# Kernel optimization log

Measured on AMD Instinct MI355X. Metric: run time of the kernel, lower is better.

Reference implementation:

```python
import jax, jax.numpy as jnp
import numpy as np
from jax import lax

B, T, C = 2, 1024, 2048
H, N = 32, 64
LAYER_ID, N_LAYER = 1, 24
EPS = 1e-5 * 64.0  # 1e-5 * head_size_divisor**2, divisor=8
RESCALE_T = 256.0 * 0.7  # bf16_limit * 0.7


def setup_inputs():
    key = jax.random.key(0)
    ks = jax.random.split(key, 16)
    r01 = LAYER_ID / (N_LAYER - 1)
    r10 = 1.0 - LAYER_ID / N_LAYER
    ddd = np.arange(C, dtype=np.float64) / C
    pw = lambda p: jnp.asarray(1.0 - ddd ** p, jnp.float32)
    n = np.arange(C, dtype=np.float64)
    decay = -7.0 + 5.0 * (n / (C - 1)) ** (0.85 + r01 ** 0.5)
    sc = lambda k, shp, s: jax.random.normal(k, shp, jnp.float32) * s
    return {
        'x': sc(ks[0], (B, T, C), 1.0),
        'v_first': sc(ks[1], (B, T, C), 1.0),
        'x_r': pw(0.2 * r10), 'x_w': pw(0.9 * r10),
        'x_k': jnp.asarray(1.0 - (ddd ** (0.9 * r10) + 0.4 * r01), jnp.float32),
        'x_v': jnp.asarray(1.0 - (ddd ** (0.4 * r10) + 0.6 * r01), jnp.float32),
        'x_a': pw(0.9 * r10), 'x_g': pw(0.2 * r10),
        'w0': jnp.asarray(decay + 0.5, jnp.float32),
        'w1': sc(ks[2], (C, 64), 0.02), 'w2': sc(ks[3], (64, C), 0.02),
        'a0': jnp.zeros((C,), jnp.float32),
        'a1': sc(ks[4], (C, 64), 0.02), 'a2': sc(ks[5], (64, C), 0.02),
        'v0': jnp.ones((C,), jnp.float32),
        'v1': sc(ks[6], (C, 32), 0.02), 'v2': sc(ks[7], (32, C), 0.02),
        'g1': sc(ks[8], (C, 128), 0.02), 'g2': sc(ks[9], (128, C), 0.02),
        'k_k': jnp.full((C,), 0.85, jnp.float32),
        'k_a': jnp.ones((C,), jnp.float32),
        'r_k': sc(ks[10], (H, N), 0.05),
        'W_r': sc(ks[11], (C, C), C ** -0.5),
        'W_k': sc(ks[12], (C, C), C ** -0.5),
        'W_v': sc(ks[13], (C, C), C ** -0.5),
        'W_o': sc(ks[14], (C, C), C ** -0.5),
        'ln_w': jnp.ones((C,), jnp.float32),
        'ln_b': jnp.zeros((C,), jnp.float32),
    }


def wkv7(r, w, k, v, a, b):
    # RWKV-7 per-head linear state recurrence: S <- S*diag(w) + S a b^T + v k^T; out = S r
    Bsz, Tlen, Cd = r.shape
    to = lambda t: t.reshape(Bsz, Tlen, H, N).transpose(1, 0, 2, 3)  # (T,B,H,N)
    rr, kk, vv, aa, bb = map(to, (r, k, v, a, b))
    ww = jnp.exp(-jnp.exp(to(w)))  # decay in (0,1); w <= -0.5 guaranteed upstream

    def step(S, xs):
        rt, wt, kt, vt, at, bt = xs
        sa = jnp.einsum('bhij,bhj->bhi', S, at)
        S = S * wt[:, :, None, :] + sa[..., None] * bt[:, :, None, :] + vt[..., None] * kt[:, :, None, :]
        return S, jnp.einsum('bhij,bhj->bhi', S, rt)

    S0 = jnp.zeros((Bsz, H, N, N), r.dtype)
    _, out = lax.scan(step, S0, (rr, ww, kk, vv, aa, bb))
    return out.transpose(1, 0, 2, 3).reshape(Bsz, Tlen, Cd)


def reference(x, v_first, x_r, x_w, x_k, x_v, x_a, x_g, w0, w1, w2, a0, a1, a2,
              v0, v1, v2, g1, g2, k_k, k_a, r_k, W_r, W_k, W_v, W_o, ln_w, ln_b):
    # token shift (ZeroPad2d((0,0,1,-1)))
    xx = jnp.concatenate([jnp.zeros_like(x[:, :1]), x[:, :-1]], axis=1) - x
    xr = x + xx * x_r; xw = x + xx * x_w; xk = x + xx * x_k
    xv = x + xx * x_v; xa = x + xx * x_a; xg = x + xx * x_g
    r = xr @ W_r.T
    w = -jax.nn.softplus(-(w0 + jnp.tanh(xw @ w1) @ w2)) - 0.5  # soft clamp to (-inf,-0.5]
    k = xk @ W_k.T
    v = xv @ W_v.T
    # layer_id > 0: value residual gated toward v_first (with max-abs rescales)
    v1p = xv @ v1
    v1p = v1p / jnp.maximum(jnp.max(jnp.abs(v1p)), 1.0)
    v2p = v1p @ v2
    v2p = v2p / jnp.maximum(jnp.max(jnp.abs(v2p)), 1.0)
    gate = jax.nn.sigmoid(jnp.clip(v0 + v2p, -16.0, 16.0))
    vd = v_first - v
    vd = vd / jnp.maximum(jnp.max(jnp.abs(vd)), 1.0)
    v = v + vd * gate
    a = jax.nn.sigmoid(a0 + (xa @ a1) @ a2)
    g = jax.nn.sigmoid(xg @ g1) @ g2
    kk = (k * k_k).reshape(B, T, H, N)
    kk = (kk / jnp.maximum(jnp.linalg.norm(kk, axis=-1, keepdims=True), 1e-12)).reshape(B, T, C)
    k = k * (1.0 + (a - 1.0) * k_a)
    y = wkv7(r, w, k, v, -kk, kk * a)
    needs_rescale = jnp.max(jnp.abs(y)) > RESCALE_T
    # GroupNorm: H groups of size N
    yg = y.reshape(B, T, H, N)
    mu = yg.mean(-1, keepdims=True)
    var = yg.var(-1, keepdims=True)
    y = ((yg - mu) / jnp.sqrt(var + EPS)).reshape(B, T, C) * ln_w + ln_b
    y = y + ((r.reshape(B, T, H, N) * k.reshape(B, T, H, N) * r_k).sum(-1, keepdims=True)
             * v.reshape(B, T, H, N)).reshape(B, T, C)
    y = (y * g) @ W_o.T
    y = jnp.where(needs_rescale, y * 0.5, y)
    v_first_out = jnp.where(needs_rescale, v_first * 0.5, v_first)
    return y, v_first_out
```

## Files before the change

### kernel.cpp

```cpp
#include <hip/hip_runtime.h>
#include <hip/hip_bf16.h>

#define ELq 4194304
#define Cq 2048
#define Tq 1024
#define Hq 32
#define Mq 2048

typedef __attribute__((ext_vector_type(8))) short bf16x8;
typedef __attribute__((ext_vector_type(4))) float f32x4;

__device__ __forceinline__ unsigned short f2bu(float f) {
  union { float f; unsigned u; } v; v.f = f;
  unsigned r = v.u + 0x7fffu + ((v.u >> 16) & 1u);
  return (unsigned short)(r >> 16);
}
__device__ __forceinline__ float b2f(unsigned short u) {
  union { unsigned u; float f; } v; v.u = ((unsigned)u) << 16;
  return v.f;
}
__device__ __forceinline__ void gl_lds16(const void* g, void* l) {
  __builtin_amdgcn_global_load_lds((const __attribute__((address_space(1))) unsigned int*)g,
                                   (__attribute__((address_space(3))) unsigned int*)l, 16, 0, 0);
}

template<int CTRL>
__device__ __forceinline__ float dpp_add(float x) {
  int t = __builtin_amdgcn_update_dpp(0, __builtin_bit_cast(int, x), CTRL, 0xF, 0xF, true);
  return x + __builtin_bit_cast(float, t);
}

struct ConvJob { const float* src; unsigned short* dst; int rows, cols, trans; };
struct ConvJobs { ConvJob j[12]; };

__global__ void k_conv(ConvJobs jobs) {
  ConvJob jb = jobs.j[blockIdx.z];
  int n = jb.rows * jb.cols;
  if (!jb.trans) {
    int n4 = n >> 2;
    for (int i = blockIdx.x * blockDim.x + threadIdx.x; i < n4; i += gridDim.x * blockDim.x) {
      float4 v = ((const float4*)jb.src)[i];
      ushort4 o;
      o.x = f2bu(v.x); o.y = f2bu(v.y); o.z = f2bu(v.z); o.w = f2bu(v.w);
      ((ushort4*)jb.dst)[i] = o;
    }
  } else {
    for (int i = blockIdx.x * blockDim.x + threadIdx.x; i < n; i += gridDim.x * blockDim.x) {
      int col = i / jb.rows;
      int row = i - col * jb.rows;
      jb.dst[i] = f2bu(jb.src[(size_t)row * jb.cols + col]);
    }
  }
}

__global__ void k_zero(unsigned int* p) { if (threadIdx.x < 8) p[threadIdx.x] = 0u; }

__global__ void k_prologue(const float* __restrict__ x,
    const float* __restrict__ mr, const float* __restrict__ mw, const float* __restrict__ mk,
    const float* __restrict__ mv, const float* __restrict__ ma, const float* __restrict__ mg,
    unsigned short* __restrict__ xr, unsigned short* __restrict__ xw, unsigned short* __restrict__ xk,
    unsigned short* __restrict__ xv, unsigned short* __restrict__ xa, unsigned short* __restrict__ xg)
{
  int i4 = blockIdx.x * 256 + threadIdx.x;
  if (i4 >= ELq / 4) return;
  int i = i4 << 2;
  float4 xc = *(const float4*)(x + i);
  int t = (i >> 11) & (Tq - 1);
  float4 xp = make_float4(0.f, 0.f, 0.f, 0.f);
  if (t) xp = *(const float4*)(x + i - Cq);
  float4 dx = make_float4(xp.x - xc.x, xp.y - xc.y, xp.z - xc.z, xp.w - xc.w);
  int c = i & (Cq - 1);
  auto mix = [&](const float* __restrict__ m, unsigned short* __restrict__ o) {
    float4 mm = *(const float4*)(m + c);
    ushort4 u;
    u.x = f2bu(xc.x + dx.x * mm.x); u.y = f2bu(xc.y + dx.y * mm.y);
    u.z = f2bu(xc.z + dx.z * mm.z); u.w = f2bu(xc.w + dx.w * mm.w);
    *(ushort4*)(o + i) = u;
  };
  mix(mr, xr); mix(mw, xw); mix(mk, xk); mix(mv, xv); mix(ma, xa); mix(mg, xg);
}

struct GJob {
  const unsigned short* A; const unsigned short* B;
  const float* bias; float* Cf; unsigned short* Cb;
  unsigned int* amax; const float* aux;
  int K; int ld; int epi;
};
struct GJobs { GJob j[4]; };

__device__ __forceinline__ void epi_store(int epi, float v, size_t o,
    float* Cf, unsigned short* Cb, const float* bias, const float* aux, int col, float& lmax)
{
  switch (epi) {
    case 0: Cf[o] = v; break;
    case 1: Cf[o] = v + bias[col]; break;
    case 2: Cf[o] = 1.f / (1.f + expf(-(v + bias[col]))); break;
    case 4: Cb[o] = f2bu(v); break;
    case 7: lmax = fmaxf(lmax, fabsf(v)); Cf[o] = v; break;
    case 9: lmax = fmaxf(lmax, fabsf(aux[o] - v)); Cf[o] = v; break;
  }
}

__global__ __launch_bounds__(256, 2) void k_gemm128(GJobs jobs) {
  GJob jb = jobs.j[blockIdx.z];
  __shared__ __align__(16) unsigned short As[128 * 32];
  __shared__ __align__(16) unsigned short Bs[128 * 32];
  __shared__ float sred[4];
  const int tid = threadIdx.x, lane = tid & 63, wid = tid >> 6;
  const int wr = wid >> 1, wc = wid & 1;
  const int lin = blockIdx.y * 16 + blockIdx.x;
  const int swz = (lin & 7) * 32 + (lin >> 3);
  const int m0 = (swz >> 4) * 128, n0 = (swz & 15) * 128;
  const int K = jb.K, ld = jb.ld;
  const unsigned short* A = jb.A; const unsigned short* B = jb.B;
  f32x4 acc[4][4] = {};
  for (int k0 = 0; k0 < K; k0 += 32) {
    #pragma unroll
    for (int i = 0; i < 2; ++i) {
      int cw = wid * 64 + i * 256;
      int c = cw + lane;
      int row = c >> 2, q = c & 3;
      gl_lds16(A + (size_t)(m0 + row) * ld + k0 + q * 8, &As[cw * 8]);
      gl_lds16(B + (size_t)(n0 + row) * ld + k0 + q * 8, &Bs[cw * 8]);
    }
    __syncthreads();
    const int kg = (lane >> 4) * 8;
    bf16x8 af[4], bq[4];
    #pragma unroll
    for (int mi = 0; mi < 4; ++mi)
      af[mi] = *(const bf16x8*)&As[(wr * 64 + mi * 16 + (lane & 15)) * 32 + kg];
    #pragma unroll
    for (int ni = 0; ni < 4; ++ni)
      bq[ni] = *(const bf16x8*)&Bs[(wc * 64 + ni * 16 + (lane & 15)) * 32 + kg];
    #pragma unroll
    for (int mi = 0; mi < 4; ++mi)
      #pragma unroll
      for (int ni = 0; ni < 4; ++ni)
        acc[mi][ni] = __builtin_amdgcn_mfma_f32_16x16x32_bf16(af[mi], bq[ni], acc[mi][ni], 0, 0, 0);
    __syncthreads();
  }
  float lmax = 0.f;
  #pragma unroll
  for (int mi = 0; mi < 4; ++mi)
    #pragma unroll
    for (int ni = 0; ni < 4; ++ni) {
      int col = n0 + wc * 64 + ni * 16 + (lane & 15);
      int row = m0 + wr * 64 + mi * 16 + ((lane >> 4) << 2);
      #pragma unroll
      for (int q = 0; q < 4; ++q)
        epi_store(jb.epi, acc[mi][ni][q], (size_t)(row + q) * 2048 + col,
                  jb.Cf, jb.Cb, jb.bias, jb.aux, col, lmax);
    }
  if (jb.epi == 7 || jb.epi == 9) {
    #pragma unroll
    for (int o = 32; o; o >>= 1) lmax = fmaxf(lmax, __shfl_xor(lmax, o));
    if (lane == 0) sred[wid] = lmax;
    __syncthreads();
    if (tid == 0)
      atomicMax(jb.amax, __float_as_uint(fmaxf(fmaxf(sred[0], sred[1]), fmaxf(sred[2], sred[3]))));
  }
}

template<int TBN>
__global__ __launch_bounds__(256, 2) void k_gemmN_sk(GJob jb) {
  __shared__ __align__(16) unsigned short As[128 * 32];
  __shared__ __align__(16) unsigned short Bs[TBN * 32];
  const int tid = threadIdx.x, lane = tid & 63, wid = tid >> 6;
  const int m0 = blockIdx.x * 128;
  const int koff = blockIdx.y * 256;
  const int ld = jb.ld;
  constexpr int NF = TBN / 16;
  const unsigned short* A = jb.A + koff;
  const unsigned short* B = jb.B + koff;
  float* out = jb.Cf + (size_t)blockIdx.y * (2048 * TBN);
  f32x4 acc[2][NF] = {};
  for (int k0 = 0; k0 < 256; k0 += 32) {
    for (int cw = wid * 64; cw < 512; cw += 256) {
      int c = cw + lane; int row = c >> 2, q = c & 3;
      gl_lds16(A + (size_t)(m0 + row) * ld + k0 + q * 8, &As[cw * 8]);
    }
    for (int cw = wid * 64; cw < TBN * 4; cw += 256) {
      int c = cw + lane; int row = c >> 2, q = c & 3;
      gl_lds16(B + (size_t)row * ld + k0 + q * 8, &Bs[cw * 8]);
    }
    __syncthreads();
    const int kg = (lane >> 4) * 8;
    bf16x8 af[2], bq[NF];
    #pragma unroll
    for (int mi = 0; mi < 2; ++mi)
      af[mi] = *(const bf16x8*)&As[(wid * 32 + mi * 16 + (lane & 15)) * 32 + kg];
    #pragma unroll
    for (int ni = 0; ni < NF; ++ni)
      bq[ni] = *(const bf16x8*)&Bs[(ni * 16 + (lane & 15)) * 32 + kg];
    #pragma unroll
    for (int mi = 0; mi < 2; ++mi)
      #pragma unroll
      for (int ni = 0; ni < NF; ++ni)
        acc[mi][ni] = __builtin_amdgcn_mfma_f32_16x16x32_bf16(af[mi], bq[ni], acc[mi][ni], 0, 0, 0);
    __syncthreads();
  }
  #pragma unroll
  for (int mi = 0; mi < 2; ++mi)
    #pragma unroll
    for (int ni = 0; ni < NF; ++ni) {
      int col = ni * 16 + (lane & 15);
      int row = m0 + wid * 32 + mi * 16 + ((lane >> 4) << 2);
      #pragma unroll
      for (int q = 0; q < 4; ++q)
        out[(size_t)(row + q) * TBN + col] = acc[mi][ni][q];
    }
}

__global__ void k_skepi(const float* __restrict__ pw, const float* __restrict__ pa,
                        const float* __restrict__ pv, const float* __restrict__ pg,
                        unsigned short* __restrict__ hw, unsigned short* __restrict__ ha,
                        unsigned short* __restrict__ hv, unsigned short* __restrict__ hg,
                        unsigned int* __restrict__ amax) {
  int i = blockIdx.x * 256 + threadIdx.x;
  const float* src; unsigned short* dst; int stride, mode, loc;
  if (i < 131072)      { src = pw; dst = hw; stride = 131072; mode = 0; loc = i; }
  else if (i < 262144) { src = pa; dst = ha; stride = 131072; mode = 1; loc = i - 131072; }
  else if (i < 327680) { src = pv; dst = hv; stride = 65536;  mode = 2; loc = i - 262144; }
  else                 { src = pg; dst = hg; stride = 262144; mode = 3; loc = i - 327680; }
  float s = 0.f;
  #pragma unroll
  for (int sp = 0; sp < 8; ++sp) s += src[loc + (size_t)sp * stride];
  float lmax = 0.f, o;
  switch (mode) {
    case 0: o = tanhf(s); break;
    case 1: o = s; break;
    case 2: o = s; lmax = fabsf(s); break;
    default: o = 1.f / (1.f + expf(-s)); break;
  }
  dst[loc] = f2bu(o);
  #pragma unroll
  for (int of = 32; of; of >>= 1) lmax = fmaxf(lmax, __shfl_xor(lmax, of));
  if ((threadIdx.x & 63) == 0 && lmax > 0.f) atomicMax(amax, __float_as_uint(lmax));
}

__global__ __launch_bounds__(256) void k_vprep(float* __restrict__ v, const float* __restrict__ vf,
    const float* __restrict__ z, const float* __restrict__ v0c, const unsigned int* __restrict__ sc,
    float* __restrict__ k, float* __restrict__ w, float* __restrict__ asig, float* __restrict__ kkout,
    const float* __restrict__ kkw, const float* __restrict__ kaw) {
  int wid = threadIdx.x >> 6, lane = threadIdx.x & 63;
  int idx = blockIdx.x * 4 + wid;
  size_t off = (size_t)idx * 64 + lane;
  int c = ((idx & (Hq - 1)) << 6) | lane;
  float m1 = fmaxf(__uint_as_float(sc[0]), 1.f);
  float m2 = fmaxf(__uint_as_float(sc[1]) / m1, 1.f);
  float mvd = fmaxf(__uint_as_float(sc[2]), 1.f);
  float gx = v0c[c] + z[off] / (m1 * m2);
  gx = fminf(fmaxf(gx, -16.f), 16.f);
  float gate = 1.f / (1.f + expf(-gx));
  float vr = v[off];
  v[off] = vr + (vf[off] - vr) * (gate / mvd);
  float kr = k[off];
  float kkv = kr * kkw[c];
  float ss = kkv * kkv;
  #pragma unroll
  for (int o = 32; o; o >>= 1) ss += __shfl_xor(ss, o);
  float kkn = kkv / fmaxf(sqrtf(ss), 1e-12f);
  float as = asig[off];
  kkout[off] = -kkn;
  asig[off] = kkn * as;
  k[off] = kr * (1.f + (as - 1.f) * kaw[c]);
  float wl = w[off];
  float wlog = -log1pf(expf(-wl)) - 0.5f;
  w[off] = expf(-expf(wlog));
}

struct SRg { float4 r0, r1, w0, w1, k0, k1, a0, a1, b0, b1; float v; };

__device__ __forceinline__ void ld_g(SRg& R,
    const float* __restrict__ rS, const float* __restrict__ wS, const float* __restrict__ kS,
    const float* __restrict__ vS, const float* __restrict__ aS, const float* __restrict__ bS,
    size_t sb, int cq8, int row) {
  R.r0 = *(const float4*)(rS + sb + cq8); R.r1 = *(const float4*)(rS + sb + cq8 + 4);
  R.w0 = *(const float4*)(wS + sb + cq8); R.w1 = *(const float4*)(wS + sb + cq8 + 4);
  R.k0 = *(const float4*)(kS + sb + cq8); R.k1 = *(const float4*)(kS + sb + cq8 + 4);
  R.a0 = *(const float4*)(aS + sb + cq8); R.a1 = *(const float4*)(aS + sb + cq8 + 4);
  R.b0 = *(const float4*)(bS + sb + cq8); R.b1 = *(const float4*)(bS + sb + cq8 + 4);
  R.v  = vS[sb + row];
}

__device__ __forceinline__ void wkv_step(const SRg& R, float S[8], float& ymx,
    float* __restrict__ y, size_t yoff, int lane) {
  float sa = (S[0]*R.a0.x + S[1]*R.a0.y) + (S[2]*R.a0.z + S[3]*R.a0.w)
           + (S[4]*R.a1.x + S[5]*R.a1.y) + (S[6]*R.a1.z + S[7]*R.a1.w);
  sa = dpp_add<0xB1>(sa);
  sa = dpp_add<0x4E>(sa);
  sa = dpp_add<0x141>(sa);
  float vi = R.v;
  float s0 = S[0]*R.w0.x + (sa*R.b0.x + vi*R.k0.x);
  float s1 = S[1]*R.w0.y + (sa*R.b0.y + vi*R.k0.y);
  float s2 = S[2]*R.w0.z + (sa*R.b0.z + vi*R.k0.z);
  float s3 = S[3]*R.w0.w + (sa*R.b0.w + vi*R.k0.w);
  float s4 = S[4]*R.w1.x + (sa*R.b1.x + vi*R.k1.x);
  float s5 = S[5]*R.w1.y + (sa*R.b1.y + vi*R.k1.y);
  float s6 = S[6]*R.w1.z + (sa*R.b1.z + vi*R.k1.z);
  float s7 = S[7]*R.w1.w + (sa*R.b1.w + vi*R.k1.w);
  S[0]=s0; S[1]=s1; S[2]=s2; S[3]=s3; S[4]=s4; S[5]=s5; S[6]=s6; S[7]=s7;
  float yp = (s0*R.r0.x + s1*R.r0.y) + (s2*R.r0.z + s3*R.r0.w)
           + (s4*R.r1.x + s5*R.r1.y) + (s6*R.r1.z + s7*R.r1.w);
  yp = dpp_add<0xB1>(yp);
  yp = dpp_add<0x4E>(yp);
  yp = dpp_add<0x141>(yp);
  if ((lane & 7) == 0) {
    y[yoff] = yp;
    ymx = fmaxf(ymx, fabsf(yp));
  }
}

__global__ __launch_bounds__(64, 1) void k_wkv(
    const float* __restrict__ rS, const float* __restrict__ wS, const float* __restrict__ kS,
    const float* __restrict__ vS, const float* __restrict__ aS, const float* __restrict__ bS,
    float* __restrict__ y, unsigned int* __restrict__ ymax) {
  const int lane = threadIdx.x;
  const int bh = blockIdx.x & 63;
  const int rq = blockIdx.x >> 6;
  const int row = rq * 8 + (lane >> 3);
  const int cq8 = (lane & 7) * 8;
  float S[8];
  #pragma unroll
  for (int q = 0; q < 8; ++q) S[q] = 0.f;
  const size_t base0 = (size_t)(bh >> 5) * Tq * Cq + (size_t)(bh & 31) * 64;

  SRg R0, R1, R2, R3;
  ld_g(R0, rS, wS, kS, vS, aS, bS, base0,            cq8, row);
  ld_g(R1, rS, wS, kS, vS, aS, bS, base0 + Cq,       cq8, row);
  ld_g(R2, rS, wS, kS, vS, aS, bS, base0 + 2 * Cq,   cq8, row);
  ld_g(R3, rS, wS, kS, vS, aS, bS, base0 + 3 * Cq,   cq8, row);

  float ymx = 0.f;
  for (int t = 0; t < Tq; t += 4) {
    int t4 = (t + 4 < Tq) ? t + 4 : Tq - 1;
    int t5 = (t + 5 < Tq) ? t + 5 : Tq - 1;
    int t6 = (t + 6 < Tq) ? t + 6 : Tq - 1;
    int t7 = (t + 7 < Tq) ? t + 7 : Tq - 1;
    wkv_step(R0, S, ymx, y, base0 + (size_t)t * Cq + row, lane);
    ld_g(R0, rS, wS, kS, vS, aS, bS, base0 + (size_t)t4 * Cq, cq8, row);
    wkv_step(R1, S, ymx, y, base0 + (size_t)(t + 1) * Cq + row, lane);
    ld_g(R1, rS, wS, kS, vS, aS, bS, base0 + (size_t)t5 * Cq, cq8, row);
    wkv_step(R2, S, ymx, y, base0 + (size_t)(t + 2) * Cq + row, lane);
    ld_g(R2, rS, wS, kS, vS, aS, bS, base0 + (size_t)t6 * Cq, cq8, row);
    wkv_step(R3, S, ymx, y, base0 + (size_t)(t + 3) * Cq + row, lane);
    ld_g(R3, rS, wS, kS, vS, aS, bS, base0 + (size_t)t7 * Cq, cq8, row);
  }
  #pragma unroll
  for (int o = 32; o; o >>= 1) ymx = fmaxf(ymx, __shfl_xor(ymx, o));
  if (lane == 0) atomicMax(ymax, __float_as_uint(ymx));
}

__global__ __launch_bounds__(256) void k_epi1(const float* __restrict__ y, const float* __restrict__ r,
    const float* __restrict__ k, const float* __restrict__ v, const unsigned short* __restrict__ g,
    const float* __restrict__ lnw, const float* __restrict__ lnb, const float* __restrict__ rk,
    unsigned short* __restrict__ yg) {
  int wid = threadIdx.x >> 6, lane = threadIdx.x & 63;
  int idx = blockIdx.x * 4 + wid;
  size_t off = (size_t)idx * 64 + lane;
  int c = ((idx & (Hq - 1)) << 6) | lane;
  float yv = y[off];
  float s = yv;
  #pragma unroll
  for (int o = 32; o; o >>= 1) s += __shfl_xor(s, o);
  float mu = s * (1.f / 64.f);
  float d = yv - mu;
  float vs = d * d;
  #pragma unroll
  for (int o = 32; o; o >>= 1) vs += __shfl_xor(vs, o);
  float yn = d / sqrtf(vs * (1.f / 64.f) + 6.4e-4f);
  float yo = yn * lnw[c] + lnb[c];
  float bon = r[off] * k[off] * rk[c];
  #pragma unroll
  for (int o = 32; o; o >>= 1) bon += __shfl_xor(bon, o);
  yo += bon * v[off];
  yg[off] = f2bu(yo * b2f(g[off]));
}

__global__ void k_wo_fin(const float* __restrict__ p0, const float* __restrict__ p1,
                         const unsigned int* __restrict__ sc, float* __restrict__ out) {
  int i = blockIdx.x * 256 + threadIdx.x;
  if (i >= ELq / 4) return;
  float s = (__uint_as_float(sc[3]) > 179.2f) ? 0.5f : 1.f;
  float4 a = ((const float4*)p0)[i];
  float4 b = ((const float4*)p1)[i];
  ((float4*)out)[i] = make_float4((a.x + b.x) * s, (a.y + b.y) * s,
                                  (a.z + b.z) * s, (a.w + b.w) * s);
}

__global__ void k_vout(const float* __restrict__ vf, const unsigned int* __restrict__ sc,
                       float* __restrict__ out) {
  int i = blockIdx.x * 256 + threadIdx.x;
  if (i >= ELq) return;
  float s = (__uint_as_float(sc[3]) > 179.2f) ? 0.5f : 1.f;
  out[i] = vf[i] * s;
}

extern "C" void kernel_launch(void* const* d_in, const int* in_sizes, int n_in,
                              void* d_out, int out_size, void* d_ws, size_t ws_size,
                              hipStream_t stream) {
  const float* x      = (const float*)d_in[0];
  const float* vfirst = (const float*)d_in[1];
  const float* x_r = (const float*)d_in[2];
  const float* x_w = (const float*)d_in[3];
  const float* x_k = (const float*)d_in[4];
  const float* x_v = (const float*)d_in[5];
  const float* x_a = (const float*)d_in[6];
  const float* x_g = (const float*)d_in[7];
  const float* w0 = (const float*)d_in[8];
  const float* w1 = (const float*)d_in[9];
  const float* w2 = (const float*)d_in[10];
  const float* a0 = (const float*)d_in[11];
  const float* a1 = (const float*)d_in[12];
  const float* a2 = (const float*)d_in[13];
  const float* v0 = (const float*)d_in[14];
  const float* v1 = (const float*)d_in[15];
  const float* v2 = (const float*)d_in[16];
  const float* g1 = (const float*)d_in[17];
  const float* g2 = (const float*)d_in[18];
  const float* k_k = (const float*)d_in[19];
  const float* k_a = (const float*)d_in[20];
  const float* r_k = (const float*)d_in[21];
  const float* W_r = (const float*)d_in[22];
  const float* W_k = (const float*)d_in[23];
  const float* W_v = (const float*)d_in[24];
  const float* W_o = (const float*)d_in[25];
  const float* lnw = (const float*)d_in[26];
  const float* lnb = (const float*)d_in[27];

  char* ws = (char*)d_ws;
  size_t off = 0;
  auto alloc = [&](size_t bytes) -> void* {
    void* p = ws + off; off += (bytes + 255) & ~(size_t)255; return p;
  };
  unsigned int* scal = (unsigned int*)alloc(256);
  float* kbuf  = (float*)alloc((size_t)ELq * 4);
  float* vbuf  = (float*)alloc((size_t)ELq * 4);
  float* wbuf  = (float*)alloc((size_t)ELq * 4);
  float* abuf  = (float*)alloc((size_t)ELq * 4);
  float* kkbuf = (float*)alloc((size_t)ELq * 4);
  float* ybuf  = (float*)alloc((size_t)ELq * 4);
  unsigned short* xrb = (unsigned short*)alloc((size_t)ELq * 2);
  unsigned short* xwb = (unsigned short*)alloc((size_t)ELq * 2);
  unsigned short* xkb = (unsigned short*)alloc((size_t)ELq * 2);
  unsigned short* xvb = (unsigned short*)alloc((size_t)ELq * 2);
  unsigned short* xab = (unsigned short*)alloc((size_t)ELq * 2);
  unsigned short* xgb = (unsigned short*)alloc((size_t)ELq * 2);
  unsigned short* gbuf = (unsigned short*)alloc((size_t)ELq * 2);
  unsigned short* ygb  = (unsigned short*)alloc((size_t)ELq * 2);
  unsigned short* WrB = (unsigned short*)alloc((size_t)ELq * 2);
  unsigned short* WkB = (unsigned short*)alloc((size_t)ELq * 2);
  unsigned short* WvB = (unsigned short*)alloc((size_t)ELq * 2);
  unsigned short* WoB = (unsigned short*)alloc((size_t)ELq * 2);
  unsigned short* w1T = (unsigned short*)alloc(64 * 2048 * 2);
  unsigned short* a1T = (unsigned short*)alloc(64 * 2048 * 2);
  unsigned short* v1T = (unsigned short*)alloc(32 * 2048 * 2);
  unsigned short* g1T = (unsigned short*)alloc(128 * 2048 * 2);
  unsigned short* w2T = (unsigned short*)alloc(2048 * 64 * 2);
  unsigned short* a2T = (unsigned short*)alloc(2048 * 64 * 2);
  unsigned short* v2T = (unsigned short*)alloc(2048 * 32 * 2);
  unsigned short* g2T = (unsigned short*)alloc(2048 * 128 * 2);
  unsigned short* hwb = (unsigned short*)alloc((size_t)Mq * 64 * 2);
  unsigned short* hab = (unsigned short*)alloc((size_t)Mq * 64 * 2);
  unsigned short* hvb = (unsigned short*)alloc((size_t)Mq * 32 * 2);
  unsigned short* hgb = (unsigned short*)alloc((size_t)Mq * 128 * 2);
  float* pskw = (float*)alloc((size_t)8 * Mq * 64 * 4);
  float* pska = (float*)alloc((size_t)8 * Mq * 64 * 4);
  float* pskv = (float*)alloc((size_t)8 * Mq * 32 * 4);
  float* pskg = (float*)alloc((size_t)8 * Mq * 128 * 4);
  float* rbuf = (float*)d_out;
  float* zbuf = (float*)d_out + ELq;
  float* yout = (float*)d_out;
  float* vfout = (float*)d_out + ELq;
  float* pWo0 = (float*)xrb;
  float* pWo1 = pWo0 + ELq;

  k_zero<<<1, 64, 0, stream>>>(scal);

  ConvJobs cj;
  cj.j[0]  = {W_r, WrB, Cq, Cq, 0};
  cj.j[1]  = {W_k, WkB, Cq, Cq, 0};
  cj.j[2]  = {W_v, WvB, Cq, Cq, 0};
  cj.j[3]  = {W_o, WoB, Cq, Cq, 0};
  cj.j[4]  = {w1, w1T, 2048, 64, 1};
  cj.j[5]  = {a1, a1T, 2048, 64, 1};
  cj.j[6]  = {v1, v1T, 2048, 32, 1};
  cj.j[7]  = {g1, g1T, 2048, 128, 1};
  cj.j[8]  = {w2, w2T, 64, 2048, 1};
  cj.j[9]  = {a2, a2T, 64, 2048, 1};
  cj.j[10] = {v2, v2T, 32, 2048, 1};
  cj.j[11] = {g2, g2T, 128, 2048, 1};
  k_conv<<<dim3(1024, 1, 12), 256, 0, stream>>>(cj);

  k_prologue<<<ELq / 1024, 256, 0, stream>>>(x, x_r, x_w, x_k, x_v, x_a, x_g,
                                             xrb, xwb, xkb, xvb, xab, xgb);

  GJobs g1j;
  g1j.j[0] = {xrb, WrB, nullptr, rbuf, nullptr, nullptr, nullptr, 2048, 2048, 0};
  g1j.j[1] = {xkb, WkB, nullptr, kbuf, nullptr, nullptr, nullptr, 2048, 2048, 0};
  g1j.j[2] = {xvb, WvB, nullptr, vbuf, nullptr, scal + 2, vfirst, 2048, 2048, 9};
  g1j.j[3] = g1j.j[0];
  k_gemm128<<<dim3(16, 16, 3), 256, 0, stream>>>(g1j);

  GJob jw = {xwb, w1T, nullptr, pskw, nullptr, nullptr, nullptr, 256, 2048, 0};
  k_gemmN_sk<64><<<dim3(16, 8), 256, 0, stream>>>(jw);
  GJob ja = {xab, a1T, nullptr, pska, nullptr, nullptr, nullptr, 256, 2048, 0};
  k_gemmN_sk<64><<<dim3(16, 8), 256, 0, stream>>>(ja);
  GJob jv = {xvb, v1T, nullptr, pskv, nullptr, nullptr, nullptr, 256, 2048, 0};
  k_gemmN_sk<32><<<dim3(16, 8), 256, 0, stream>>>(jv);
  GJob jg = {xgb, g1T, nullptr, pskg, nullptr, nullptr, nullptr, 256, 2048, 0};
  k_gemmN_sk<128><<<dim3(16, 8), 256, 0, stream>>>(jg);
  k_skepi<<<2304, 256, 0, stream>>>(pskw, pska, pskv, pskg, hwb, hab, hvb, hgb, scal + 0);

  GJobs g3j;
  g3j.j[0] = {hwb, w2T, w0, wbuf, nullptr, nullptr, nullptr, 64, 64, 1};
  g3j.j[1] = {hab, a2T, a0, abuf, nullptr, nullptr, nullptr, 64, 64, 2};
  g3j.j[2] = {hvb, v2T, nullptr, zbuf, nullptr, scal + 1, nullptr, 32, 32, 7};
  g3j.j[3] = {hgb, g2T, nullptr, nullptr, gbuf, nullptr, nullptr, 128, 128, 4};
  k_gemm128<<<dim3(16, 16, 4), 256, 0, stream>>>(g3j);

  k_vprep<<<(2 * Tq * Hq) / 4, 256, 0, stream>>>(vbuf, vfirst, zbuf, v0, scal,
                                                 kbuf, wbuf, abuf, kkbuf, k_k, k_a);
  k_wkv<<<8 * 2 * Hq, 64, 0, stream>>>(rbuf, wbuf, kbuf, vbuf, kkbuf, abuf, ybuf, scal + 3);
  k_epi1<<<(2 * Tq * Hq) / 4, 256, 0, stream>>>(ybuf, rbuf, kbuf, vbuf, gbuf, lnw, lnb, r_k, ygb);

  GJobs gfj;
  gfj.j[0] = {ygb, WoB, nullptr, pWo0, nullptr, nullptr, nullptr, 1024, 2048, 0};
  gfj.j[1] = {ygb + 1024, WoB + 1024, nullptr, pWo1, nullptr, nullptr, nullptr, 1024, 2048, 0};
  gfj.j[2] = gfj.j[0]; gfj.j[3] = gfj.j[0];
  k_gemm128<<<dim3(16, 16, 2), 256, 0, stream>>>(gfj);
  k_wo_fin<<<ELq / 1024, 256, 0, stream>>>(pWo0, pWo1, scal, yout);

  k_vout<<<ELq / 256, 256, 0, stream>>>(vfirst, scal, vfout);
}
```

Baseline: 531.7 us.

## Fuse k/w preprocessing into GEMM epilogues and split WKV state across more lanes

Moves the decay transform into the small w2 GEMM epilogue and the kk normalization, a-scaling and k update into the W_k GEMM epilogue. To make this possible the big GEMM now launches after the LoRA GEMMs. The standalone vprep kernel shrinks to a vectorized v-gating kernel, which removes several full-tensor read/write passes. The WKV kernel now gives each lane 4 state columns with a 16-lane reduction and launches twice as many blocks, trading extra DPP steps per timestep for more parallelism and shorter per-lane work.

```diff
diff --git a/kernel.cpp b/kernel.cpp
--- a/kernel.cpp
+++ b/kernel.cpp
@@ -85,6 +85,7 @@
   const float* bias; float* Cf; unsigned short* Cb;
   unsigned int* amax; const float* aux;
   int K; int ld; int epi;
+  float* kkp; float* abp; const float* kkw; const float* kaw;
 };
 struct GJobs { GJob j[4]; };
 
@@ -98,6 +99,12 @@
     case 4: Cb[o] = f2bu(v); break;
     case 7: lmax = fmaxf(lmax, fabsf(v)); Cf[o] = v; break;
     case 9: lmax = fmaxf(lmax, fabsf(aux[o] - v)); Cf[o] = v; break;
+    case 10: {
+      float wv = v + bias[col];
+      float wlog = -log1pf(expf(-wv)) - 0.5f;
+      Cf[o] = expf(-expf(wlog));
+      break;
+    }
   }
 }
 
@@ -138,6 +145,42 @@
       for (int ni = 0; ni < 4; ++ni)
         acc[mi][ni] = __builtin_amdgcn_mfma_f32_16x16x32_bf16(af[mi], bq[ni], acc[mi][ni], 0, 0, 0);
     __syncthreads();
+  }
+  if (jb.epi == 11) {
+    float kkwv[4], kawv[4]; int colv[4];
+    #pragma unroll
+    for (int ni = 0; ni < 4; ++ni) {
+      colv[ni] = n0 + wc * 64 + ni * 16 + (lane & 15);
+      kkwv[ni] = jb.kkw[colv[ni]];
+      kawv[ni] = jb.kaw[colv[ni]];
+    }
+    #pragma unroll
+    for (int mi = 0; mi < 4; ++mi) {
+      #pragma unroll
+      for (int q = 0; q < 4; ++q) {
+        float kkv[4]; float ss = 0.f;
+        #pragma unroll
+        for (int ni = 0; ni < 4; ++ni) {
+          kkv[ni] = acc[mi][ni][q] * kkwv[ni];
+          ss += kkv[ni] * kkv[ni];
+        }
+        ss = dpp_add<0xB1>(ss); ss = dpp_add<0x4E>(ss);
+        ss = dpp_add<0x141>(ss); ss = dpp_add<0x140>(ss);
+        float inv = 1.f / fmaxf(sqrtf(ss), 1e-12f);
+        int row = m0 + wr * 64 + mi * 16 + ((lane >> 4) << 2) + q;
+        #pragma unroll
+        for (int ni = 0; ni < 4; ++ni) {
+          size_t o = (size_t)row * 2048 + colv[ni];
+          float kraw = acc[mi][ni][q];
+          float kkn = kkv[ni] * inv;
+          float as = jb.abp[o];
+          jb.kkp[o] = -kkn;
+          jb.abp[o] = kkn * as;
+          jb.Cf[o] = kraw * (1.f + (as - 1.f) * kawv[ni]);
+        }
+      }
+    }
+    return;
   }
   float lmax = 0.f;
   #pragma unroll
@@ -238,74 +281,66 @@
   if ((threadIdx.x & 63) == 0 && lmax > 0.f) atomicMax(amax, __float_as_uint(lmax));
 }
 
-__global__ __launch_bounds__(256) void k_vprep(float* __restrict__ v, const float* __restrict__ vf,
-    const float* __restrict__ z, const float* __restrict__ v0c, const unsigned int* __restrict__ sc,
-    float* __restrict__ k, float* __restrict__ w, float* __restrict__ asig, float* __restrict__ kkout,
-    const float* __restrict__ kkw, const float* __restrict__ kaw) {
-  int wid = threadIdx.x >> 6, lane = threadIdx.x & 63;
-  int idx = blockIdx.x * 4 + wid;
-  size_t off = (size_t)idx * 64 + lane;
-  int c = ((idx & (Hq - 1)) << 6) | lane;
+__global__ void k_vfin(float* __restrict__ v, const float* __restrict__ vf,
+                       const float* __restrict__ z, const float* __restrict__ v0c,
+                       const unsigned int* __restrict__ sc) {
+  int i4 = blockIdx.x * 256 + threadIdx.x;
+  if (i4 >= ELq / 4) return;
+  int i = i4 << 2;
   float m1 = fmaxf(__uint_as_float(sc[0]), 1.f);
   float m2 = fmaxf(__uint_as_float(sc[1]) / m1, 1.f);
-  float mvd = fmaxf(__uint_as_float(sc[2]), 1.f);
-  float gx = v0c[c] + z[off] / (m1 * m2);
-  gx = fminf(fmaxf(gx, -16.f), 16.f);
-  float gate = 1.f / (1.f + expf(-gx));
-  float vr = v[off];
-  v[off] = vr + (vf[off] - vr) * (gate / mvd);
-  float kr = k[off];
-  float kkv = kr * kkw[c];
-  float ss = kkv * kkv;
-  #pragma unroll
-  for (int o = 32; o; o >>= 1) ss += __shfl_xor(ss, o);
-  float kkn = kkv / fmaxf(sqrtf(ss), 1e-12f);
-  float as = asig[off];
-  kkout[off] = -kkn;
-  asig[off] = kkn * as;
-  k[off] = kr * (1.f + (as - 1.f) * kaw[c]);
-  float wl = w[off];
-  float wlog = -log1pf(expf(-wl)) - 0.5f;
-  w[off] = expf(-expf(wlog));
-}
-
-struct SRg { float4 r0, r1, w0, w1, k0, k1, a0, a1, b0, b1; float v; };
+  float inv12 = 1.f / (m1 * m2);
+  float invvd = 1.f / fmaxf(__uint_as_float(sc[2]), 1.f);
+  int c = i & (Cq - 1);
+  float4 zv = *(const float4*)(z + i);
+  float4 vv = *(const float4*)(v + i);
+  float4 fv = *(const float4*)(vf + i);
+  float4 v0v = *(const float4*)(v0c + c);
+  float4 o;
+  #pragma unroll
+  for (int j = 0; j < 4; ++j) {
+    float gx = (&v0v.x)[j] + (&zv.x)[j] * inv12;
+    gx = fminf(fmaxf(gx, -16.f), 16.f);
+    float gate = 1.f / (1.f + expf(-gx));
+    float vr = (&vv.x)[j];
+    (&o.x)[j] = vr + ((&fv.x)[j] - vr) * (gate * invvd);
+  }
+  *(float4*)(v + i) = o;
+}
+
+struct SRg { float4 r, w, k, a, b; float v; };
 
 __device__ __forceinline__ void ld_g(SRg& R,
     const float* __restrict__ rS, const float* __restrict__ wS, const float* __restrict__ kS,
     const float* __restrict__ vS, const float* __restrict__ aS, const float* __restrict__ bS,
-    size_t sb, int cq8, int row) {
-  R.r0 = *(const float4*)(rS + sb + cq8); R.r1 = *(const float4*)(rS + sb + cq8 + 4);
-  R.w0 = *(const float4*)(wS + sb + cq8); R.w1 = *(const float4*)(wS + sb + cq8 + 4);
-  R.k0 = *(const float4*)(kS + sb + cq8); R.k1 = *(const float4*)(kS + sb + cq8 + 4);
-  R.a0 = *(const float4*)(aS + sb + cq8); R.a1 = *(const float4*)(aS + sb + cq8 + 4);
-  R.b0 = *(const float4*)(bS + sb + cq8); R.b1 = *(const float4*)(bS + sb + cq8 + 4);
-  R.v  = vS[sb + row];
-}
-
-__device__ __forceinline__ void wkv_step(const SRg& R, float S[8], float& ymx,
+    size_t sb, int cl, int row) {
+  R.r = *(const float4*)(rS + sb + cl);
+  R.w = *(const float4*)(wS + sb + cl);
+  R.k = *(const float4*)(kS + sb + cl);
+  R.a = *(const float4*)(aS + sb + cl);
+  R.b = *(const float4*)(bS + sb + cl);
+  R.v = vS[sb + row];
+}
+
+__device__ __forceinline__ void wkv_step(const SRg& R, float S[4], float& ymx,
     float* __restrict__ y, size_t yoff, int lane) {
-  float sa = (S[0]*R.a0.x + S[1]*R.a0.y) + (S[2]*R.a0.z + S[3]*R.a0.w)
-           + (S[4]*R.a1.x + S[5]*R.a1.y) + (S[6]*R.a1.z + S[7]*R.a1.w);
+  float sa = (S[0]*R.a.x + S[1]*R.a.y) + (S[2]*R.a.z + S[3]*R.a.w);
   sa = dpp_add<0xB1>(sa);
   sa = dpp_add<0x4E>(sa);
   sa = dpp_add<0x141>(sa);
+  sa = dpp_add<0x140>(sa);
   float vi = R.v;
-  float s0 = S[0]*R.w0.x + (sa*R.b0.x + vi*R.k0.x);
-  float s1 = S[1]*R.w0.y + (sa*R.b0.y + vi*R.k0.y);
-  float s2 = S[2]*R.w0.z + (sa*R.b0.z + vi*R.k0.z);
-  float s3 = S[3]*R.w0.w + (sa*R.b0.w + vi*R.k0.w);
-  float s4 = S[4]*R.w1.x + (sa*R.b1.x + vi*R.k1.x);
-  float s5 = S[5]*R.w1.y + (sa*R.b1.y + vi*R.k1.y);
-  float s6 = S[6]*R.w1.z + (sa*R.b1.z + vi*R.k1.z);
-  float s7 = S[7]*R.w1.w + (sa*R.b1.w + vi*R.k1.w);
-  S[0]=s0; S[1]=s1; S[2]=s2; S[3]=s3; S[4]=s4; S[5]=s5; S[6]=s6; S[7]=s7;
-  float yp = (s0*R.r0.x + s1*R.r0.y) + (s2*R.r0.z + s3*R.r0.w)
-           + (s4*R.r1.x + s5*R.r1.y) + (s6*R.r1.z + s7*R.r1.w);
+  float s0 = S[0]*R.w.x + (sa*R.b.x + vi*R.k.x);
+  float s1 = S[1]*R.w.y + (sa*R.b.y + vi*R.k.y);
+  float s2 = S[2]*R.w.z + (sa*R.b.z + vi*R.k.z);
+  float s3 = S[3]*R.w.w + (sa*R.b.w + vi*R.k.w);
+  S[0]=s0; S[1]=s1; S[2]=s2; S[3]=s3;
+  float yp = (s0*R.r.x + s1*R.r.y) + (s2*R.r.z + s3*R.r.w);
   yp = dpp_add<0xB1>(yp);
   yp = dpp_add<0x4E>(yp);
   yp = dpp_add<0x141>(yp);
-  if ((lane & 7) == 0) {
+  yp = dpp_add<0x140>(yp);
+  if ((lane & 15) == 0) {
     y[yoff] = yp;
     ymx = fmaxf(ymx, fabsf(yp));
   }
@@ -318,18 +353,18 @@
   const int lane = threadIdx.x;
   const int bh = blockIdx.x & 63;
   const int rq = blockIdx.x >> 6;
-  const int row = rq * 8 + (lane >> 3);
-  const int cq8 = (lane & 7) * 8;
-  float S[8];
-  #pragma unroll
-  for (int q = 0; q < 8; ++q) S[q] = 0.f;
+  const int row = rq * 4 + (lane >> 4);
+  const int cl = (lane & 15) * 4;
+  float S[4];
+  #pragma unroll
+  for (int q = 0; q < 4; ++q) S[q] = 0.f;
   const size_t base0 = (size_t)(bh >> 5) * Tq * Cq + (size_t)(bh & 31) * 64;
 
   SRg R0, R1, R2, R3;
-  ld_g(R0, rS, wS, kS, vS, aS, bS, base0,            cq8, row);
-  ld_g(R1, rS, wS, kS, vS, aS, bS, base0 + Cq,       cq8, row);
-  ld_g(R2, rS, wS, kS, vS, aS, bS, base0 + 2 * Cq,   cq8, row);
-  ld_g(R3, rS, wS, kS, vS, aS, bS, base0 + 3 * Cq,   cq8, row);
+  ld_g(R0, rS, wS, kS, vS, aS, bS, base0,          cl, row);
+  ld_g(R1, rS, wS, kS, vS, aS, bS, base0 + Cq,     cl, row);
+  ld_g(R2, rS, wS, kS, vS, aS, bS, base0 + 2 * Cq, cl, row);
+  ld_g(R3, rS, wS, kS, vS, aS, bS, base0 + 3 * Cq, cl, row);
 
   float ymx = 0.f;
   for (int t = 0; t < Tq; t += 4) {
@@ -338,13 +373,13 @@
     int t6 = (t + 6 < Tq) ? t + 6 : Tq - 1;
     int t7 = (t + 7 < Tq) ? t + 7 : Tq - 1;
     wkv_step(R0, S, ymx, y, base0 + (size_t)t * Cq + row, lane);
-    ld_g(R0, rS, wS, kS, vS, aS, bS, base0 + (size_t)t4 * Cq, cq8, row);
+    ld_g(R0, rS, wS, kS, vS, aS, bS, base0 + (size_t)t4 * Cq, cl, row);
     wkv_step(R1, S, ymx, y, base0 + (size_t)(t + 1) * Cq + row, lane);
-    ld_g(R1, rS, wS, kS, vS, aS, bS, base0 + (size_t)t5 * Cq, cq8, row);
+    ld_g(R1, rS, wS, kS, vS, aS, bS, base0 + (size_t)t5 * Cq, cl, row);
     wkv_step(R2, S, ymx, y, base0 + (size_t)(t + 2) * Cq + row, lane);
-    ld_g(R2, rS, wS, kS, vS, aS, bS, base0 + (size_t)t6 * Cq, cq8, row);
+    ld_g(R2, rS, wS, kS, vS, aS, bS, base0 + (size_t)t6 * Cq, cl, row);
     wkv_step(R3, S, ymx, y, base0 + (size_t)(t + 3) * Cq + row, lane);
-    ld_g(R3, rS, wS, kS, vS, aS, bS, base0 + (size_t)t7 * Cq, cq8, row);
+    ld_g(R3, rS, wS, kS, vS, aS, bS, base0 + (size_t)t7 * Cq, cl, row);
   }
   #pragma unroll
   for (int o = 32; o; o >>= 1) ymx = fmaxf(ymx, __shfl_xor(ymx, o));
@@ -495,13 +530,6 @@
   k_prologue<<<ELq / 1024, 256, 0, stream>>>(x, x_r, x_w, x_k, x_v, x_a, x_g,
                                              xrb, xwb, xkb, xvb, xab, xgb);
 
-  GJobs g1j;
-  g1j.j[0] = {xrb, WrB, nullptr, rbuf, nullptr, nullptr, nullptr, 2048, 2048, 0};
-  g1j.j[1] = {xkb, WkB, nullptr, kbuf, nullptr, nullptr, nullptr, 2048, 2048, 0};
-  g1j.j[2] = {xvb, WvB, nullptr, vbuf, nullptr, scal + 2, vfirst, 2048, 2048, 9};
-  g1j.j[3] = g1j.j[0];
-  k_gemm128<<<dim3(16, 16, 3), 256, 0, stream>>>(g1j);
-
   GJob jw = {xwb, w1T, nullptr, pskw, nullptr, nullptr, nullptr, 256, 2048, 0};
   k_gemmN_sk<64><<<dim3(16, 8), 256, 0, stream>>>(jw);
   GJob ja = {xab, a1T, nullptr, pska, nullptr, nullptr, nullptr, 256, 2048, 0};
@@ -513,15 +541,22 @@
   k_skepi<<<2304, 256, 0, stream>>>(pskw, pska, pskv, pskg, hwb, hab, hvb, hgb, scal + 0);
 
   GJobs g3j;
-  g3j.j[0] = {hwb, w2T, w0, wbuf, nullptr, nullptr, nullptr, 64, 64, 1};
+  g3j.j[0] = {hwb, w2T, w0, wbuf, nullptr, nullptr, nullptr, 64, 64, 10};
   g3j.j[1] = {hab, a2T, a0, abuf, nullptr, nullptr, nullptr, 64, 64, 2};
   g3j.j[2] = {hvb, v2T, nullptr, zbuf, nullptr, scal + 1, nullptr, 32, 32, 7};
   g3j.j[3] = {hgb, g2T, nullptr, nullptr, gbuf, nullptr, nullptr, 128, 128, 4};
   k_gemm128<<<dim3(16, 16, 4), 256, 0, stream>>>(g3j);
 
-  k_vprep<<<(2 * Tq * Hq) / 4, 256, 0, stream>>>(vbuf, vfirst, zbuf, v0, scal,
-                                                 kbuf, wbuf, abuf, kkbuf, k_k, k_a);
-  k_wkv<<<8 * 2 * Hq, 64, 0, stream>>>(rbuf, wbuf, kbuf, vbuf, kkbuf, abuf, ybuf, scal + 3);
+  GJobs g1j;
+  g1j.j[0] = {xrb, WrB, nullptr, rbuf, nullptr, nullptr, nullptr, 2048, 2048, 0};
+  g1j.j[1] = {xkb, WkB, nullptr, kbuf, nullptr, nullptr, nullptr, 2048, 2048, 11,
+              kkbuf, abuf, k_k, k_a};
+  g1j.j[2] = {xvb, WvB, nullptr, vbuf, nullptr, scal + 2, vfirst, 2048, 2048, 9};
+  g1j.j[3] = g1j.j[0];
+  k_gemm128<<<dim3(16, 16, 3), 256, 0, stream>>>(g1j);
+
+  k_vfin<<<ELq / 1024, 256, 0, stream>>>(vbuf, vfirst, zbuf, v0, scal);
+  k_wkv<<<16 * 2 * Hq, 64, 0, stream>>>(rbuf, wbuf, kbuf, vbuf, kkbuf, abuf, ybuf, scal + 3);
   k_epi1<<<(2 * Tq * Hq) / 4, 256, 0, stream>>>(ybuf, rbuf, kbuf, vbuf, gbuf, lnw, lnb, r_k, ygb);
 
   GJobs gfj;
```

Result: slower. 551.3 us (+3.7%).
